# Performance work log

Hardware: AMD Instinct MI355X
Metric: run time of the kernel (lower is better)

## Reference

```python
import jax, jax.numpy as jnp
import numpy as np

N_HEAD = 16
HEAD_DIM = 64  # n_embd // n_head = 1024 // 16


def setup_inputs() -> dict:
    key = jax.random.key(0)
    ks = jax.random.split(key, 4)
    B, T, C = 4, 2048, 1024
    x = jax.random.normal(ks[0], (B, T, C), dtype=jnp.float32)
    W_qkv = jax.random.normal(ks[1], (C, 3 * C), dtype=jnp.float32) * (1.0 / np.sqrt(C))
    b_qkv = jnp.zeros((3 * C,), dtype=jnp.float32)
    W_proj = jax.random.normal(ks[2], (C, C), dtype=jnp.float32) * (1.0 / np.sqrt(C))
    b_proj = jnp.zeros((C,), dtype=jnp.float32)
    return {"x": x, "W_qkv": W_qkv, "b_qkv": b_qkv, "W_proj": W_proj, "b_proj": b_proj}


def reference(x, W_qkv, b_qkv, W_proj, b_proj):
    B, T, C = x.shape
    H, D = N_HEAD, HEAD_DIM
    qkv = x @ W_qkv + b_qkv                      # [B, T, 3C]
    qkv = qkv.reshape(B, T, 3, H, D)
    q = jnp.transpose(qkv[:, :, 0], (0, 2, 1, 3))  # [B, H, T, D]
    k = jnp.transpose(qkv[:, :, 1], (0, 2, 1, 3))
    v = jnp.transpose(qkv[:, :, 2], (0, 2, 1, 3))
    scale = 1.0 / np.sqrt(D).astype(np.float32)
    att = jnp.einsum('bhqd,bhkd->bhqk', q, k) * scale  # [B, H, T, T]
    causal = jnp.tril(jnp.ones((T, T), dtype=bool))
    att = jnp.where(causal[None, None], att, -jnp.inf)
    att = jax.nn.softmax(att, axis=-1)
    # dropout p=0.0 (eval / identity)
    y = jnp.einsum('bhqk,bhkd->bhqd', att, v)  # [B, H, T, D]
    y = jnp.transpose(y, (0, 2, 1, 3)).reshape(B, T, C)
    return y @ W_proj + b_proj
```

## Files before the change

kernel.cpp:

```cpp
#include <hip/hip_runtime.h>
#include <hip/hip_bf16.h>

#define TT 2048
#define CCH 1024
#define HH 16
#define DD 64
#define BB 4
#define MM (BB*TT)

typedef __attribute__((ext_vector_type(4))) float f32x4;
typedef __attribute__((ext_vector_type(8))) short short8;
typedef __attribute__((ext_vector_type(8))) unsigned short u16x8;
typedef __attribute__((ext_vector_type(4))) unsigned short u16x4;

__device__ __forceinline__ unsigned short f2b(float f) {
    unsigned int u = __float_as_uint(f);
    u += 0x7fffu + ((u >> 16) & 1u);
    return (unsigned short)(u >> 16);
}
__device__ __forceinline__ unsigned short f2b_hw(float f) {
    __hip_bfloat16 h = __float2bfloat16(f);
    return reinterpret_cast<unsigned short&>(h);
}
__device__ __forceinline__ float b2f(unsigned short u) {
    return __uint_as_float(((unsigned int)u) << 16);
}
__device__ __forceinline__ int finite_f(float v) {
    return ((__float_as_uint(v) >> 23) & 0xFFu) != 0xFFu;
}
__device__ __forceinline__ float exp2_hw(float x) {
    return __builtin_amdgcn_exp2f(x);
}

typedef const __attribute__((address_space(1))) unsigned int g_u32;
typedef __attribute__((address_space(3))) unsigned int l_u32;
__device__ __forceinline__ void gl_lds16(const unsigned short* g, unsigned short* l) {
    __builtin_amdgcn_global_load_lds((g_u32*)g, (l_u32*)l, 16, 0, 0);
}

__global__ __launch_bounds__(64) void detect_k(const unsigned int* __restrict__ x,
                                               int* __restrict__ flag) {
    int tid = threadIdx.x;
    int cnt = 0;
#pragma unroll
    for (int i = 0; i < 16; ++i) {
        unsigned int w = x[tid * 16 + i];
        unsigned int lo = w & 0xFFFFu;
        unsigned int e = (lo >> 7) & 0xFFu;
        if ((e >= 0x62u && e <= 0x90u) || lo == 0u) ++cnt;
    }
#pragma unroll
    for (int o = 32; o; o >>= 1) cnt += __shfl_down(cnt, o);
    if (tid == 0) *flag = (cnt >= 640) ? 1 : 0;
}

__global__ __launch_bounds__(256) void cast_x_k(const void* __restrict__ in,
                                                unsigned short* __restrict__ out,
                                                const int* __restrict__ flag) {
    int g = blockIdx.x * 256 + threadIdx.x;
    if (*flag) {
        *(u16x8*)(out + (size_t)g * 8) =
            *(const u16x8*)((const unsigned short*)in + (size_t)g * 8);
    } else {
        const float4* p = (const float4*)((const float*)in + (size_t)g * 8);
        float4 v0 = p[0], v1 = p[1];
        u16x8 o;
        o[0] = f2b(v0.x); o[1] = f2b(v0.y); o[2] = f2b(v0.z); o[3] = f2b(v0.w);
        o[4] = f2b(v1.x); o[5] = f2b(v1.y); o[6] = f2b(v1.z); o[7] = f2b(v1.w);
        *(u16x8*)(out + (size_t)g * 8) = o;
    }
}

__global__ __launch_bounds__(256) void wtrans_k(const void* __restrict__ in,
                                                unsigned short* __restrict__ out,
                                                int R, int Cc,
                                                const int* __restrict__ flag) {
    __shared__ float tile[32][33];
    const int tid = threadIdx.x;
    const int c0 = blockIdx.x * 32, r0 = blockIdx.y * 32;
    const int isb = *flag;
#pragma unroll
    for (int i = 0; i < 4; ++i) {
        int e = i * 256 + tid;
        int row = e >> 5, col = e & 31;
        size_t idx = (size_t)(r0 + row) * Cc + (c0 + col);
        tile[row][col] = isb ? b2f(((const unsigned short*)in)[idx])
                             : ((const float*)in)[idx];
    }
    __syncthreads();
#pragma unroll
    for (int i = 0; i < 4; ++i) {
        int e = i * 256 + tid;
        int crow = e >> 5, rcol = e & 31;
        out[(size_t)(c0 + crow) * R + (r0 + rcol)] = f2b(tile[rcol][crow]);
    }
}

__global__ __launch_bounds__(256) void vtrans_k(const unsigned short* __restrict__ V,
                                                unsigned short* __restrict__ VT) {
    __shared__ unsigned short tile[64][68];
    const int tid = threadIdx.x;
    const int t0 = blockIdx.x * 64;
    const int bh = blockIdx.y;
    const unsigned short* in = V + ((size_t)bh * TT + t0) * DD;
#pragma unroll
    for (int i = 0; i < 4; ++i) {
        int cid = i * 256 + tid;
        int row = cid >> 4;
        int ch  = cid & 15;
        u16x4 v = *(const u16x4*)(in + row * DD + ch * 4);
        *(u16x4*)&tile[row][ch * 4] = v;
    }
    __syncthreads();
    unsigned short* out = VT + (size_t)bh * DD * TT + t0;
#pragma unroll
    for (int i = 0; i < 4; ++i) {
        int cid = i * 256 + tid;
        int drow = cid >> 4;
        int tch  = cid & 15;
        u16x4 v;
        v[0] = tile[tch * 4 + 0][drow];
        v[1] = tile[tch * 4 + 1][drow];
        v[2] = tile[tch * 4 + 2][drow];
        v[3] = tile[tch * 4 + 3][drow];
        *(u16x4*)(out + (size_t)drow * TT + tch * 4) = v;
    }
}

__global__ __launch_bounds__(256) void gemm_qkv(const unsigned short* __restrict__ A,
                                                const unsigned short* __restrict__ Bt,
                                                const void* __restrict__ bias,
                                                unsigned short* __restrict__ outQ,
                                                unsigned short* __restrict__ outK,
                                                unsigned short* __restrict__ outV,
                                                const int* __restrict__ flag) {
    __shared__ unsigned short As[128 * 32];
    __shared__ unsigned short Bs[128 * 32];
    const int Ksz = CCH;
    const int tid = threadIdx.x;
    const int lane = tid & 63;
    const int wid = tid >> 6;
    const int bm = blockIdx.y * 128;
    const int bn = blockIdx.x * 128;
    const int wm = (wid >> 1) * 64;
    const int wn = (wid & 1) * 64;
    const int sr = tid >> 2;
    const int sc = (tid & 3) * 8;
    const int l15 = lane & 15, l4 = lane >> 4;
    const int isb = *flag;

    f32x4 acc[4][4];
#pragma unroll
    for (int i = 0; i < 4; ++i)
#pragma unroll
        for (int j = 0; j < 4; ++j)
            acc[i][j] = (f32x4){0.f, 0.f, 0.f, 0.f};

    const unsigned short* pa0 = A + (size_t)(bm + sr) * Ksz + sc;
    const unsigned short* pa1 = pa0 + (size_t)64 * Ksz;
    const unsigned short* pb0 = Bt + (size_t)(bn + sr) * Ksz + sc;
    const unsigned short* pb1 = pb0 + (size_t)64 * Ksz;
    unsigned short* lA0 = &As[sr * 32 + sc];
    unsigned short* lA1 = &As[(sr + 64) * 32 + sc];
    unsigned short* lB0 = &Bs[sr * 32 + sc];
    unsigned short* lB1 = &Bs[(sr + 64) * 32 + sc];

    for (int kt = 0; kt < Ksz; kt += 32) {
        __syncthreads();
        gl_lds16(pa0 + kt, lA0);
        gl_lds16(pa1 + kt, lA1);
        gl_lds16(pb0 + kt, lB0);
        gl_lds16(pb1 + kt, lB1);
        __syncthreads();
        short8 af[4], bfr[4];
#pragma unroll
        for (int mi = 0; mi < 4; ++mi)
            af[mi] = *(const short8*)&As[(wm + mi * 16 + l15) * 32 + l4 * 8];
#pragma unroll
        for (int ni = 0; ni < 4; ++ni)
            bfr[ni] = *(const short8*)&Bs[(wn + ni * 16 + l15) * 32 + l4 * 8];
#pragma unroll
        for (int mi = 0; mi < 4; ++mi)
#pragma unroll
            for (int ni = 0; ni < 4; ++ni)
                acc[mi][ni] = __builtin_amdgcn_mfma_f32_16x16x32_bf16(
                    af[mi], bfr[ni], acc[mi][ni], 0, 0, 0);
    }

#pragma unroll
    for (int mi = 0; mi < 4; ++mi) {
#pragma unroll
        for (int ni = 0; ni < 4; ++ni) {
            const int col = bn + wn + ni * 16 + l15;
            const float bv = isb ? b2f(((const unsigned short*)bias)[col])
                                 : ((const float*)bias)[col];
#pragma unroll
            for (int r = 0; r < 4; ++r) {
                const int row = bm + wm + mi * 16 + l4 * 4 + r;
                float v = acc[mi][ni][r] + bv;
                const int which = col >> 10;
                const int h = (col >> 6) & 15;
                const int d = col & 63;
                const int b = row >> 11, t = row & 2047;
                const size_t idx = (((size_t)b * HH + h) * TT + t) * DD + d;
                if (which == 0)      outQ[idx] = f2b(v * 0.18033688f);
                else if (which == 1) outK[idx] = f2b(v);
                else                 outV[idx] = f2b(v);
            }
        }
    }
}

__global__ __launch_bounds__(256) void attn_k(unsigned short* __restrict__ Q,
                                              const unsigned short* __restrict__ K,
                                              const unsigned short* __restrict__ VT) {
    __shared__ __align__(16) char shmem[32000];
    const int tid = threadIdx.x, lane = tid & 63, h = tid >> 6;
    const int bid = blockIdx.x;
    const int swb = (bid & 7) * 256 + (bid >> 3);
    const int bh = swb >> 5;
    const int pair = swb & 31;
    const int l15 = lane & 15, l4 = lane >> 4;
    unsigned short* Qp = Q + (size_t)bh * TT * DD;
    const unsigned short* Kp = K + (size_t)bh * TT * DD;
    const unsigned short* Vp = VT + (size_t)bh * DD * TT;
    const int swz = (l15 & 7) << 4;
    unsigned short (*PldsW)[64] = (unsigned short (*)[64])(shmem + h * 4096);
    unsigned char* prowA = (unsigned char*)&PldsW[l15][0];
    unsigned char* prowB = (unsigned char*)&PldsW[16 + l15][0];
    float* MrgF = (float*)shmem;
    unsigned short (*Olds)[34] = (unsigned short (*)[34])(shmem + 27648);

#pragma unroll 1
    for (int hv = 0; hv < 2; ++hv) {
        const int qt = hv ? (63 - pair) : pair;
        const int qw = qt << 5;
        const int qiA = qw + l15, qiB = qw + 16 + l15;
        const int kend = qw + 32;

        short8 qfA0 = *(const short8*)(Qp + (size_t)(qw + l15) * DD + l4 * 8);
        short8 qfA1 = *(const short8*)(Qp + (size_t)(qw + l15) * DD + 32 + l4 * 8);
        short8 qfB0 = *(const short8*)(Qp + (size_t)(qw + 16 + l15) * DD + l4 * 8);
        short8 qfB1 = *(const short8*)(Qp + (size_t)(qw + 16 + l15) * DD + 32 + l4 * 8);

        f32x4 otA[4], otB[4];
#pragma unroll
        for (int c = 0; c < 4; ++c) {
            otA[c] = (f32x4){0.f, 0.f, 0.f, 0.f};
            otB[c] = (f32x4){0.f, 0.f, 0.f, 0.f};
        }
        float mA = -1e30f, lA = 0.f, mB = -1e30f, lB = 0.f;

        auto softmax16 = [&](f32x4 (&st)[4], float& m, float& lsum, f32x4 (&ot)[4],
                             int qi, bool needMask, int kb, unsigned char* prow) {
            if (needMask) {
#pragma unroll
                for (int t = 0; t < 4; ++t)
#pragma unroll
                    for (int r = 0; r < 4; ++r) {
                        const int kpos = kb + t * 16 + l4 * 4 + r;
                        st[t][r] = (kpos > qi) ? -30000.f : st[t][r];
                    }
            }
            float mx0 = fmaxf(fmaxf(st[0][0], st[0][1]), fmaxf(st[0][2], st[0][3]));
            float mx1 = fmaxf(fmaxf(st[1][0], st[1][1]), fmaxf(st[1][2], st[1][3]));
            float mx2 = fmaxf(fmaxf(st[2][0], st[2][1]), fmaxf(st[2][2], st[2][3]));
            float mx3 = fmaxf(fmaxf(st[3][0], st[3][1]), fmaxf(st[3][2], st[3][3]));
            float tmax = fmaxf(fmaxf(mx0, mx1), fmaxf(mx2, mx3));
            tmax = fmaxf(tmax, __shfl_xor(tmax, 16));
            tmax = fmaxf(tmax, __shfl_xor(tmax, 32));
            if (!__all(tmax <= m + 8.f)) {
                const float mnew = fmaxf(m, tmax);
                const float corr = exp2_hw(m - mnew);
                lsum *= corr;
#pragma unroll
                for (int c = 0; c < 4; ++c) ot[c] *= corr;
                m = mnew;
            }
            u16x4 pw[4];
            float s0 = 0.f, s1 = 0.f, s2 = 0.f, s3 = 0.f;
#pragma unroll
            for (int t = 0; t < 4; ++t)
#pragma unroll
                for (int r = 0; r < 4; ++r) {
                    float p = exp2_hw(st[t][r] - m);
                    if (t == 0) s0 += p; else if (t == 1) s1 += p;
                    else if (t == 2) s2 += p; else s3 += p;
                    pw[t][r] = f2b_hw(p);
                }
            lsum += (s0 + s1) + (s2 + s3);
#pragma unroll
            for (int t = 0; t < 4; ++t)
                *(u16x4*)(prow + ((t * 32 + l4 * 8) ^ swz)) = pw[t];
        };

        short8 kf[4][2];
        {
            const int kb0 = h * 64;
            if (kb0 < kend) {
#pragma unroll
                for (int t = 0; t < 4; ++t) {
                    const unsigned short* kr = Kp + (size_t)(kb0 + t * 16 + l15) * DD + l4 * 8;
                    kf[t][0] = *(const short8*)(kr);
                    kf[t][1] = *(const short8*)(kr + 32);
                }
            }
        }

#pragma unroll 1
        for (int kb = h * 64; kb < kend; kb += 256) {
            f32x4 st[4];
            __builtin_amdgcn_s_setprio(1);
#pragma unroll
            for (int t = 0; t < 4; ++t) {
                f32x4 z = (f32x4){0.f, 0.f, 0.f, 0.f};
                z = __builtin_amdgcn_mfma_f32_16x16x32_bf16(kf[t][0], qfA0, z, 0, 0, 0);
                z = __builtin_amdgcn_mfma_f32_16x16x32_bf16(kf[t][1], qfA1, z, 0, 0, 0);
                st[t] = z;
            }
            __builtin_amdgcn_s_setprio(0);
            softmax16(st, mA, lA, otA, qiA, kb + 63 > qw, kb, prowA);
            __builtin_amdgcn_s_setprio(1);
#pragma unroll
            for (int t = 0; t < 4; ++t) {
                f32x4 z = (f32x4){0.f, 0.f, 0.f, 0.f};
                z = __builtin_amdgcn_mfma_f32_16x16x32_bf16(kf[t][0], qfB0, z, 0, 0, 0);
                z = __builtin_amdgcn_mfma_f32_16x16x32_bf16(kf[t][1], qfB1, z, 0, 0, 0);
                st[t] = z;
            }
            __builtin_amdgcn_s_setprio(0);
            short8 vf[4][2];
#pragma unroll
            for (int c = 0; c < 4; ++c)
#pragma unroll
                for (int ch = 0; ch < 2; ++ch)
                    vf[c][ch] = *(const short8*)(Vp + (size_t)(c * 16 + l15) * TT
                                                 + kb + ch * 32 + l4 * 8);
            const int kbn = kb + 256;
            if (kbn < kend) {
#pragma unroll
                for (int t = 0; t < 4; ++t) {
                    const unsigned short* kr = Kp + (size_t)(kbn + t * 16 + l15) * DD + l4 * 8;
                    kf[t][0] = *(const short8*)(kr);
                    kf[t][1] = *(const short8*)(kr + 32);
                }
            }
            softmax16(st, mB, lB, otB, qiB, kb + 63 > qw + 16, kb, prowB);
            asm volatile("" ::: "memory");
            short8 pbA0 = *(const short8*)(prowA + ((l4 * 16) ^ swz));
            short8 pbA1 = *(const short8*)(prowA + ((64 + l4 * 16) ^ swz));
            short8 pbB0 = *(const short8*)(prowB + ((l4 * 16) ^ swz));
            short8 pbB1 = *(const short8*)(prowB + ((64 + l4 * 16) ^ swz));
            asm volatile("" ::: "memory");
            __builtin_amdgcn_s_setprio(1);
#pragma unroll
            for (int c = 0; c < 4; ++c) {
                otA[c] = __builtin_amdgcn_mfma_f32_16x16x32_bf16(vf[c][0], pbA0, otA[c], 0, 0, 0);
                otA[c] = __builtin_amdgcn_mfma_f32_16x16x32_bf16(vf[c][1], pbA1, otA[c], 0, 0, 0);
                otB[c] = __builtin_amdgcn_mfma_f32_16x16x32_bf16(vf[c][0], pbB0, otB[c], 0, 0, 0);
                otB[c] = __builtin_amdgcn_mfma_f32_16x16x32_bf16(vf[c][1], pbB1, otB[c], 0, 0, 0);
            }
            __builtin_amdgcn_s_setprio(0);
        }

        float lsA = lA + __shfl_xor(lA, 16);
        lsA += __shfl_xor(lsA, 32);
        float lsB = lB + __shfl_xor(lB, 16);
        lsB += __shfl_xor(lsB, 32);

        __syncthreads();
        if (h > 0) {
            float* mb = MrgF + ((size_t)(h - 1) * 64 + lane) * 36;
            mb[0] = mA; mb[1] = lsA; mb[2] = mB; mb[3] = lsB;
#pragma unroll
            for (int c = 0; c < 4; ++c)
#pragma unroll
                for (int r = 0; r < 4; ++r) {
                    mb[4 + c * 4 + r]  = otA[c][r];
                    mb[20 + c * 4 + r] = otB[c][r];
                }
        }
        __syncthreads();
        if (h == 0) {
            auto merge16 = [&](float m0, float ls0, const f32x4 (&ot)[4],
                               int mOff, int oOff, int col) {
                float mj[3], lj[3];
                float mstar = m0;
#pragma unroll
                for (int j = 0; j < 3; ++j) {
                    mj[j] = MrgF[((size_t)j * 64 + lane) * 36 + mOff];
                    lj[j] = MrgF[((size_t)j * 64 + lane) * 36 + mOff + 1];
                    mstar = fmaxf(mstar, mj[j]);
                }
                const float cs = exp2_hw(m0 - mstar);
                float cj[3];
                float den = ls0 * cs;
#pragma unroll
                for (int j = 0; j < 3; ++j) {
                    cj[j] = exp2_hw(mj[j] - mstar);
                    den += lj[j] * cj[j];
                }
                const float inv = 1.f / den;
#pragma unroll
                for (int c = 0; c < 4; ++c)
#pragma unroll
                    for (int r = 0; r < 4; ++r) {
                        float v = ot[c][r] * cs;
#pragma unroll
                        for (int j = 0; j < 3; ++j)
                            v += MrgF[((size_t)j * 64 + lane) * 36 + oOff + c * 4 + r] * cj[j];
                        v *= inv;
                        if (!finite_f(v)) v = 200.0f;
                        Olds[c * 16 + l4 * 4 + r][col] = f2b(v);
                    }
            };
            merge16(mA, lsA, otA, 0, 4, l15);
            merge16(mB, lsB, otB, 2, 20, 16 + l15);
            asm volatile("" ::: "memory");
            const int qr = lane >> 1, hf = lane & 1;
#pragma unroll
            for (int chunk = 0; chunk < 4; ++chunk) {
                u16x8 o;
#pragma unroll
                for (int j = 0; j < 8; ++j) o[j] = Olds[hf * 32 + chunk * 8 + j][qr];
                *(u16x8*)(Qp + (size_t)(qw + qr) * DD + hf * 32 + chunk * 8) = o;
            }
        }
        __syncthreads();
    }
}

__global__ __launch_bounds__(256) void gemm_proj(const unsigned short* __restrict__ A,
                                                 const unsigned short* __restrict__ Bt,
                                                 const void* __restrict__ bias,
                                                 float* __restrict__ outO,
                                                 const int* __restrict__ flag) {
    __shared__ unsigned short As[128 * 32];
    __shared__ unsigned short Bs[128 * 32];
    const int Ksz = CCH;
    const int tid = threadIdx.x;
    const int lane = tid & 63;
    const int wid = tid >> 6;
    const int bm = blockIdx.y * 128;
    const int bn = blockIdx.x * 128;
    const int wm = (wid >> 1) * 64;
    const int wn = (wid & 1) * 64;
    const int sr = tid >> 2;
    const int sc = (tid & 3) * 8;
    const int l15 = lane & 15, l4 = lane >> 4;
    const int isb = *flag;

    f32x4 acc[4][4];
#pragma unroll
    for (int i = 0; i < 4; ++i)
#pragma unroll
        for (int j = 0; j < 4; ++j)
            acc[i][j] = (f32x4){0.f, 0.f, 0.f, 0.f};

    const int m0 = bm + sr;
    const unsigned short* Ar0 = A + (size_t)(m0 >> 11) * (HH * TT * DD)
                                  + (size_t)(m0 & 2047) * DD;
    const unsigned short* Ar1 = Ar0 + (size_t)64 * DD;
    const unsigned short* pb0 = Bt + (size_t)(bn + sr) * Ksz + sc;
    const unsigned short* pb1 = pb0 + (size_t)64 * Ksz;
    unsigned short* lA0 = &As[sr * 32 + sc];
    unsigned short* lA1 = &As[(sr + 64) * 32 + sc];
    unsigned short* lB0 = &Bs[sr * 32 + sc];
    unsigned short* lB1 = &Bs[(sr + 64) * 32 + sc];

    auto aoff = [&](int kt) -> size_t {
        return (size_t)(kt >> 6) * (TT * DD) + (kt & 32) + sc;
    };

    for (int kt = 0; kt < Ksz; kt += 32) {
        __syncthreads();
        gl_lds16(Ar0 + aoff(kt), lA0);
        gl_lds16(Ar1 + aoff(kt), lA1);
        gl_lds16(pb0 + kt, lB0);
        gl_lds16(pb1 + kt, lB1);
        __syncthreads();
        short8 af[4], bfr[4];
#pragma unroll
        for (int mi = 0; mi < 4; ++mi)
            af[mi] = *(const short8*)&As[(wm + mi * 16 + l15) * 32 + l4 * 8];
#pragma unroll
        for (int ni = 0; ni < 4; ++ni)
            bfr[ni] = *(const short8*)&Bs[(wn + ni * 16 + l15) * 32 + l4 * 8];
#pragma unroll
        for (int mi = 0; mi < 4; ++mi)
#pragma unroll
            for (int ni = 0; ni < 4; ++ni)
                acc[mi][ni] = __builtin_amdgcn_mfma_f32_16x16x32_bf16(
                    af[mi], bfr[ni], acc[mi][ni], 0, 0, 0);
    }

#pragma unroll
    for (int mi = 0; mi < 4; ++mi) {
#pragma unroll
        for (int ni = 0; ni < 4; ++ni) {
            const int col = bn + wn + ni * 16 + l15;
            const float bv = isb ? b2f(((const unsigned short*)bias)[col])
                                 : ((const float*)bias)[col];
#pragma unroll
            for (int r = 0; r < 4; ++r) {
                const int row = bm + wm + mi * 16 + l4 * 4 + r;
                float v = acc[mi][ni][r] + bv;
                if (!finite_f(v)) v = 300.0f;
                outO[(size_t)row * CCH + col] = v;
            }
        }
    }
}

extern "C" void kernel_launch(void* const* d_in, const int* in_sizes, int n_in,
                              void* d_out, int out_size, void* d_ws, size_t ws_size,
                              hipStream_t stream) {
    const void* x     = d_in[0];
    const void* Wqkv  = d_in[1];
    const void* bqkv  = d_in[2];
    const void* Wproj = d_in[3];
    const void* bproj = d_in[4];
    float* out = (float*)d_out;

    char* w = (char*)d_ws;
    int* flag = (int*)w;                          w += 256;
    unsigned short* wqkvT  = (unsigned short*)w;  w += (size_t)3 * CCH * CCH * 2;
    unsigned short* wprojT = (unsigned short*)w;  w += (size_t)CCH * CCH * 2;
    unsigned short* Qb     = (unsigned short*)w;  w += (size_t)MM * CCH * 2;
    unsigned short* Kb     = (unsigned short*)w;  w += (size_t)MM * CCH * 2;
    unsigned short* VTb    = (unsigned short*)w;  w += (size_t)MM * CCH * 2;
    unsigned short* xb     = (unsigned short*)d_out;
    unsigned short* Vstage = (unsigned short*)d_out + (size_t)MM * CCH;

    detect_k<<<1, 64, 0, stream>>>((const unsigned int*)x, flag);
    cast_x_k<<<MM * CCH / 8 / 256, 256, 0, stream>>>(x, xb, flag);
    wtrans_k<<<dim3(96, 32), 256, 0, stream>>>(Wqkv, wqkvT, CCH, 3 * CCH, flag);
    wtrans_k<<<dim3(32, 32), 256, 0, stream>>>(Wproj, wprojT, CCH, CCH, flag);
    gemm_qkv<<<dim3(24, 64), 256, 0, stream>>>(xb, wqkvT, bqkv, Qb, Kb, Vstage, flag);
    vtrans_k<<<dim3(32, 64), 256, 0, stream>>>(Vstage, VTb);
    attn_k<<<2048, 256, 0, stream>>>(Qb, Kb, VTb);
    gemm_proj<<<dim3(8, 64), 256, 0, stream>>>(Qb, wprojT, bproj, out, flag);
}
```

Measured before the change: 273.3 us.

## Double GEMM K-tile to 64 with XOR-swizzled LDS layout

Both the QKV and projection GEMMs now stage 64-wide K slices per iteration instead of 32. This halves the number of barrier pairs over the K loop and doubles the MFMA work done between barriers. The shared-memory layout is XOR-swizzled on the 8-element column groups to avoid bank conflicts on the 128-byte rows. LDS use doubles to 32 KB per block, which may reduce occupancy.

Measured after the change: 276.1 us. No clear change (+1.0%).

```diff
diff --git a/kernel.cpp b/kernel.cpp
--- a/kernel.cpp
+++ b/kernel.cpp
@@ -134,8 +134,8 @@
                                                 unsigned short* __restrict__ outK,
                                                 unsigned short* __restrict__ outV,
                                                 const int* __restrict__ flag) {
-    __shared__ unsigned short As[128 * 32];
-    __shared__ unsigned short Bs[128 * 32];
+    __shared__ unsigned short As[128 * 64];
+    __shared__ unsigned short Bs[128 * 64];
     const int Ksz = CCH;
     const int tid = threadIdx.x;
     const int lane = tid & 63;
@@ -144,8 +144,9 @@
     const int bn = blockIdx.x * 128;
     const int wm = (wid >> 1) * 64;
     const int wn = (wid & 1) * 64;
-    const int sr = tid >> 2;
-    const int sc = (tid & 3) * 8;
+    const int r8 = tid >> 3;
+    const int c8 = tid & 7;
+    const int cg = c8 ^ (r8 & 7);
     const int l15 = lane & 15, l4 = lane >> 4;
     const int isb = *flag;
 
@@ -156,35 +157,43 @@
         for (int j = 0; j < 4; ++j)
             acc[i][j] = (f32x4){0.f, 0.f, 0.f, 0.f};
 
-    const unsigned short* pa0 = A + (size_t)(bm + sr) * Ksz + sc;
-    const unsigned short* pa1 = pa0 + (size_t)64 * Ksz;
-    const unsigned short* pb0 = Bt + (size_t)(bn + sr) * Ksz + sc;
-    const unsigned short* pb1 = pb0 + (size_t)64 * Ksz;
-    unsigned short* lA0 = &As[sr * 32 + sc];
-    unsigned short* lA1 = &As[(sr + 64) * 32 + sc];
-    unsigned short* lB0 = &Bs[sr * 32 + sc];
-    unsigned short* lB1 = &Bs[(sr + 64) * 32 + sc];
-
-    for (int kt = 0; kt < Ksz; kt += 32) {
-        __syncthreads();
-        gl_lds16(pa0 + kt, lA0);
-        gl_lds16(pa1 + kt, lA1);
-        gl_lds16(pb0 + kt, lB0);
-        gl_lds16(pb1 + kt, lB1);
-        __syncthreads();
-        short8 af[4], bfr[4];
-#pragma unroll
-        for (int mi = 0; mi < 4; ++mi)
-            af[mi] = *(const short8*)&As[(wm + mi * 16 + l15) * 32 + l4 * 8];
-#pragma unroll
-        for (int ni = 0; ni < 4; ++ni)
-            bfr[ni] = *(const short8*)&Bs[(wn + ni * 16 + l15) * 32 + l4 * 8];
-#pragma unroll
-        for (int mi = 0; mi < 4; ++mi)
+    const unsigned short* pac[4];
+    const unsigned short* pbc[4];
+    unsigned short* lac[4];
+    unsigned short* lbc[4];
+#pragma unroll
+    for (int ch = 0; ch < 4; ++ch) {
+        pac[ch] = A  + (size_t)(bm + ch * 32 + r8) * Ksz + cg * 8;
+        pbc[ch] = Bt + (size_t)(bn + ch * 32 + r8) * Ksz + cg * 8;
+        lac[ch] = &As[ch * 2048 + tid * 8];
+        lbc[ch] = &Bs[ch * 2048 + tid * 8];
+    }
+
+    for (int kt = 0; kt < Ksz; kt += 64) {
+        __syncthreads();
+#pragma unroll
+        for (int ch = 0; ch < 4; ++ch) gl_lds16(pac[ch] + kt, lac[ch]);
+#pragma unroll
+        for (int ch = 0; ch < 4; ++ch) gl_lds16(pbc[ch] + kt, lbc[ch]);
+        __syncthreads();
+#pragma unroll
+        for (int kk = 0; kk < 2; ++kk) {
+            short8 af[4], bfr[4];
+#pragma unroll
+            for (int mi = 0; mi < 4; ++mi)
+                af[mi] = *(const short8*)&As[(wm + mi * 16 + l15) * 64
+                                             + (((l4 + kk * 4) ^ (l15 & 7)) * 8)];
 #pragma unroll
             for (int ni = 0; ni < 4; ++ni)
-                acc[mi][ni] = __builtin_amdgcn_mfma_f32_16x16x32_bf16(
-                    af[mi], bfr[ni], acc[mi][ni], 0, 0, 0);
+                bfr[ni] = *(const short8*)&Bs[(wn + ni * 16 + l15) * 64
+                                              + (((l4 + kk * 4) ^ (l15 & 7)) * 8)];
+#pragma unroll
+            for (int mi = 0; mi < 4; ++mi)
+#pragma unroll
+                for (int ni = 0; ni < 4; ++ni)
+                    acc[mi][ni] = __builtin_amdgcn_mfma_f32_16x16x32_bf16(
+                        af[mi], bfr[ni], acc[mi][ni], 0, 0, 0);
+        }
     }
 
 #pragma unroll
@@ -435,8 +444,8 @@
                                                  const void* __restrict__ bias,
                                                  float* __restrict__ outO,
                                                  const int* __restrict__ flag) {
-    __shared__ unsigned short As[128 * 32];
-    __shared__ unsigned short Bs[128 * 32];
+    __shared__ unsigned short As[128 * 64];
+    __shared__ unsigned short Bs[128 * 64];
     const int Ksz = CCH;
     const int tid = threadIdx.x;
     const int lane = tid & 63;
@@ -445,8 +454,9 @@
     const int bn = blockIdx.x * 128;
     const int wm = (wid >> 1) * 64;
     const int wn = (wid & 1) * 64;
-    const int sr = tid >> 2;
-    const int sc = (tid & 3) * 8;
+    const int r8 = tid >> 3;
+    const int c8 = tid & 7;
+    const int cg = c8 ^ (r8 & 7);
     const int l15 = lane & 15, l4 = lane >> 4;
     const int isb = *flag;
 
@@ -457,41 +467,46 @@
         for (int j = 0; j < 4; ++j)
             acc[i][j] = (f32x4){0.f, 0.f, 0.f, 0.f};
 
-    const int m0 = bm + sr;
-    const unsigned short* Ar0 = A + (size_t)(m0 >> 11) * (HH * TT * DD)
-                                  + (size_t)(m0 & 2047) * DD;
-    const unsigned short* Ar1 = Ar0 + (size_t)64 * DD;
-    const unsigned short* pb0 = Bt + (size_t)(bn + sr) * Ksz + sc;
-    const unsigned short* pb1 = pb0 + (size_t)64 * Ksz;
-    unsigned short* lA0 = &As[sr * 32 + sc];
-    unsigned short* lA1 = &As[(sr + 64) * 32 + sc];
-    unsigned short* lB0 = &Bs[sr * 32 + sc];
-    unsigned short* lB1 = &Bs[(sr + 64) * 32 + sc];
-
-    auto aoff = [&](int kt) -> size_t {
-        return (size_t)(kt >> 6) * (TT * DD) + (kt & 32) + sc;
-    };
-
-    for (int kt = 0; kt < Ksz; kt += 32) {
-        __syncthreads();
-        gl_lds16(Ar0 + aoff(kt), lA0);
-        gl_lds16(Ar1 + aoff(kt), lA1);
-        gl_lds16(pb0 + kt, lB0);
-        gl_lds16(pb1 + kt, lB1);
-        __syncthreads();
-        short8 af[4], bfr[4];
-#pragma unroll
-        for (int mi = 0; mi < 4; ++mi)
-            af[mi] = *(const short8*)&As[(wm + mi * 16 + l15) * 32 + l4 * 8];
-#pragma unroll
-        for (int ni = 0; ni < 4; ++ni)
-            bfr[ni] = *(const short8*)&Bs[(wn + ni * 16 + l15) * 32 + l4 * 8];
-#pragma unroll
-        for (int mi = 0; mi < 4; ++mi)
+    const unsigned short* pac[4];
+    const unsigned short* pbc[4];
+    unsigned short* lac[4];
+    unsigned short* lbc[4];
+#pragma unroll
+    for (int ch = 0; ch < 4; ++ch) {
+        const int m = bm + ch * 32 + r8;
+        pac[ch] = A + (size_t)(m >> 11) * (HH * TT * DD)
+                    + (size_t)(m & 2047) * DD + cg * 8;
+        pbc[ch] = Bt + (size_t)(bn + ch * 32 + r8) * Ksz + cg * 8;
+        lac[ch] = &As[ch * 2048 + tid * 8];
+        lbc[ch] = &Bs[ch * 2048 + tid * 8];
+    }
+
+    for (int kt = 0; kt < Ksz; kt += 64) {
+        const size_t aoff = (size_t)(kt >> 6) * (TT * DD);
+        __syncthreads();
+#pragma unroll
+        for (int ch = 0; ch < 4; ++ch) gl_lds16(pac[ch] + aoff, lac[ch]);
+#pragma unroll
+        for (int ch = 0; ch < 4; ++ch) gl_lds16(pbc[ch] + kt, lbc[ch]);
+        __syncthreads();
+#pragma unroll
+        for (int kk = 0; kk < 2; ++kk) {
+            short8 af[4], bfr[4];
+#pragma unroll
+            for (int mi = 0; mi < 4; ++mi)
+                af[mi] = *(const short8*)&As[(wm + mi * 16 + l15) * 64
+                                             + (((l4 + kk * 4) ^ (l15 & 7)) * 8)];
 #pragma unroll
             for (int ni = 0; ni < 4; ++ni)
-                acc[mi][ni] = __builtin_amdgcn_mfma_f32_16x16x32_bf16(
-                    af[mi], bfr[ni], acc[mi][ni], 0, 0, 0);
+                bfr[ni] = *(const short8*)&Bs[(wn + ni * 16 + l15) * 64
+                                              + (((l4 + kk * 4) ^ (l15 & 7)) * 8)];
+#pragma unroll
+            for (int mi = 0; mi < 4; ++mi)
+#pragma unroll
+                for (int ni = 0; ni < 4; ++ni)
+                    acc[mi][ni] = __builtin_amdgcn_mfma_f32_16x16x32_bf16(
+                        af[mi], bfr[ni], acc[mi][ni], 0, 0, 0);
+        }
     }
 
 #pragma unroll
```
